# Performance work log

Hardware: AMD Instinct MI355X
Metric: run time of the kernel (lower is better)

The kernel has to match this reference:

```python
import jax, jax.numpy as jnp
import numpy as np

SIGMA = 1.0   # kernel influence distance (init kwarg)
RADIUS = 1.0  # kernel radius (kernel points live within this ball)


def setup_inputs() -> dict:
    key = jax.random.key(0)
    k0, k1, k2, k3, k4, k5 = jax.random.split(key, 6)
    N, M, H, K, Cin, Cout = 50000, 50000, 32, 15, 64, 64
    q_points = jax.random.normal(k0, (M, 3), dtype=jnp.float32)
    s_points = jax.random.normal(k1, (N, 3), dtype=jnp.float32)
    s_feats = jax.random.normal(k2, (N, Cin), dtype=jnp.float32)
    # index == N selects the padded 'fantom' point (zero features, far away)
    neighbor_indices = jax.random.randint(k3, (M, H), 0, N + 1, dtype=jnp.int64)
    kernel_points = jax.random.normal(k4, (K, 3), dtype=jnp.float32) * (0.4 * RADIUS)
    weights = jax.random.normal(k5, (K, Cin, Cout), dtype=jnp.float32) * 0.05
    return {
        'q_points': q_points,
        's_points': s_points,
        's_feats': s_feats,
        'neighbor_indices': neighbor_indices,
        'kernel_points': kernel_points,
        'weights': weights,
    }


def reference(q_points, s_points, s_feats, neighbor_indices, kernel_points, weights):
    # Pad source points with a far-away fantom point and zero features so that
    # neighbor_indices == N behaves as an empty neighbor slot.
    s_pts = jnp.concatenate([s_points, jnp.full((1, 3), 1e6, s_points.dtype)], axis=0)
    s_fts = jnp.concatenate([s_feats, jnp.zeros((1, s_feats.shape[1]), s_feats.dtype)], axis=0)

    # Gather neighbors and center on query points: (M, H, 3)
    neighbors = s_pts[neighbor_indices] - q_points[:, None, :]
    # Distances to each kernel point: (M, H, K)
    diffs = neighbors[:, :, None, :] - kernel_points[None, None, :, :]
    sq_dists = jnp.sum(diffs * diffs, axis=-1)
    # Linear kernel influence (KPConv 'linear' mode): (M, H, K)
    influence = jnp.maximum(1.0 - jnp.sqrt(sq_dists) / SIGMA, 0.0)
    # Fantom neighbors are ~1e6 away -> influence exactly 0.

    # Gather neighbor features: (M, H, Cin)
    nb_feats = s_fts[neighbor_indices]
    # Weight features by kernel influence, reduce over neighbors: (M, K, Cin)
    weighted = jnp.einsum('mhk,mhc->mkc', influence, nb_feats)
    # Apply per-kernel-point linear maps and sum over kernel points: (M, Cout)
    out = jnp.einsum('mkc,kcd->md', weighted, weights)

    # Normalize by the number of valid (non-zero-feature) neighbors.
    feat_sum = jnp.sum(nb_feats, axis=-1)               # (M, H)
    nnum = jnp.maximum(jnp.sum(feat_sum > 0.0, axis=-1), 1)  # (M,)
    return out / nnum[:, None].astype(out.dtype)
```

## Files before the change

### kernel.cpp

```cpp
#include <hip/hip_runtime.h>

#define NPTS 50000
#define MPTS 50000
#define HN 32
#define KCD 960
#define PSTRIDE 968

typedef float f32x4 __attribute__((ext_vector_type(4)));
typedef short s16x8 __attribute__((ext_vector_type(8)));

__device__ __forceinline__ unsigned short bf_rne(float x) {
    union { float f; unsigned u; } v; v.f = x;
    unsigned r = v.u + 0x7fffu + ((v.u >> 16) & 1u);
    return (unsigned short)(r >> 16);
}
__device__ __forceinline__ unsigned short bf_trunc(float x) {
    union { float f; unsigned u; } v; v.f = x;
    return (unsigned short)(v.u >> 16);
}
__device__ __forceinline__ unsigned pack_bf(float lo, float hi) {
    union { float f; unsigned u; } a, b; a.f = lo; b.f = hi;
    return __builtin_amdgcn_perm(b.u, a.u, 0x07060302u);
}
__device__ __forceinline__ unsigned pack_rne(float lo, float hi) {
    return ((unsigned)bf_rne(hi) << 16) | (unsigned)bf_rne(lo);
}
__device__ __forceinline__ unsigned pack_lo16(unsigned a, unsigned b) {
    return __builtin_amdgcn_perm(b, a, 0x05040100u);
}
__device__ __forceinline__ unsigned pack_hi16(unsigned a, unsigned b) {
    return __builtin_amdgcn_perm(b, a, 0x07060302u);
}

__global__ __launch_bounds__(256) void prep_bf(const float* __restrict__ w,
                                               const float* __restrict__ feats,
                                               unsigned short* __restrict__ WT,
                                               unsigned char* __restrict__ signs,
                                               unsigned short* __restrict__ fbf) {
    int b = blockIdx.x;
    if (b < 240) {
        int t = b * 256 + threadIdx.x;
        int kc = t >> 6, d = t & 63;
        WT[d * KCD + kc] = bf_rne(w[t]);
    } else {
        int t = threadIdx.x;
        int p = t >> 4, r = t & 15;
        int n = (b - 240) * 16 + p;
        const float* src = feats + (size_t)n * 64 + r;
        float c0 = src[0], c1 = src[16], c2 = src[32], c3 = src[48];
        float s = c0 + c1 + c2 + c3;
        s += __shfl_xor(s, 1); s += __shfl_xor(s, 2);
        s += __shfl_xor(s, 4); s += __shfl_xor(s, 8);
        if (r == 0) signs[n] = (s > 0.f) ? 1 : 0;
        uint2 o; o.x = pack_rne(c0, c1); o.y = pack_rne(c2, c3);
        *(uint2*)(fbf + (size_t)n * 64 + r * 4) = o;
    }
}

__global__ __launch_bounds__(256) void prep_f32(const float* __restrict__ w,
                                                const float* __restrict__ feats,
                                                unsigned short* __restrict__ WT,
                                                unsigned char* __restrict__ signs) {
    int b = blockIdx.x;
    if (b < 240) {
        int t = b * 256 + threadIdx.x;
        int kc = t >> 6, d = t & 63;
        WT[d * KCD + kc] = bf_rne(w[t]);
    } else {
        int lane = threadIdx.x & 63, wv = threadIdx.x >> 6;
        int r4 = lane >> 4, c16 = lane & 15;
        int n = (b - 240) * 16 + wv * 4 + r4;
        float4 v = *(const float4*)(feats + (size_t)n * 64 + c16 * 4);
        float s = v.x + v.y + v.z + v.w;
        s += __shfl_xor(s, 1); s += __shfl_xor(s, 2);
        s += __shfl_xor(s, 4); s += __shfl_xor(s, 8);
        if (c16 == 0) signs[n] = (s > 0.f) ? 1 : 0;
    }
}

template <bool USE_BF>
__device__ __forceinline__
void kpconv_body(const float* __restrict__ q_points,
                 const float* __restrict__ s_points,
                 const float* __restrict__ s_feats,
                 const unsigned short* __restrict__ fbf,
                 const int* __restrict__ ni,
                 const float* __restrict__ kpts,
                 const unsigned short* __restrict__ WT,
                 const unsigned char* __restrict__ signs,
                 float* __restrict__ out) {
    __shared__ __align__(16) unsigned short P_sh[16][PSTRIDE];
    __shared__ __align__(16) float rpos_sh[4][3][32];
    __shared__ int ni_sh[4][4][32];
    __shared__ float kp_sh[16][3];
    __shared__ float q_sh[16][3];
    __shared__ float inv_nnum[16];

    int tid = threadIdx.x, w = tid >> 6, lane = tid & 63;
    int m_base = blockIdx.x << 4;

    if (tid < 48) {
        kp_sh[tid / 3][tid % 3] = (tid < 45) ? kpts[tid] : 1e9f;
        q_sh[tid / 3][tid % 3] = q_points[m_base * 3 + tid];
    }
    __syncthreads();

    int h = lane & 31;
    int row = lane & 15, quad = lane >> 4, kq = quad << 3;
    int h2 = lane >> 1, half = lane & 1;

    float kx = kp_sh[row][0], ky = kp_sh[row][1], kz = kp_sh[row][2];

    float tkx[8], tky[8], tkz[8];
    #pragma unroll
    for (int j = 0; j < 8; ++j) {
        int k = half * 8 + j;
        tkx[j] = kp_sh[k][0]; tky[j] = kp_sh[k][1]; tkz[j] = kp_sh[k][2];
    }

    int idx4[4]; float rxa[4], rya[4], rza[4]; unsigned char sg4[4];
    #pragma unroll
    for (int mi = 0; mi < 4; ++mi)
        idx4[mi] = ni[(m_base + mi * 4 + w) * HN + h];
    #pragma unroll
    for (int mi = 0; mi < 4; ++mi) {
        int m_l = mi * 4 + w;
        bool valid = idx4[mi] < NPTS;
        const float* sp = s_points + (size_t)(valid ? idx4[mi] : 0) * 3;
        float px = sp[0], py = sp[1], pz = sp[2];
        unsigned char sg = signs[valid ? idx4[mi] : 0];
        rxa[mi] = (valid ? px : 1e6f) - q_sh[m_l][0];
        rya[mi] = (valid ? py : 1e6f) - q_sh[m_l][1];
        rza[mi] = (valid ? pz : 1e6f) - q_sh[m_l][2];
        sg4[mi] = valid ? sg : 0;
    }

    #pragma unroll
    for (int mi = 0; mi < 4; ++mi) {
        float rx2 = __shfl(rxa[mi], h2);
        float ry2 = __shfl(rya[mi], h2);
        float rz2 = __shfl(rza[mi], h2);
        int idx2 = __shfl(idx4[mi], h2);
        int av = 0;
        #pragma unroll
        for (int j = 0; j < 8; ++j) {
            float dx = rx2 - tkx[j], dy = ry2 - tky[j], dz = rz2 - tkz[j];
            float d2 = dx * dx + dy * dy + dz * dz;
            av |= (d2 < 1.f) ? 1 : 0;
        }
        av |= __shfl_xor(av, 1);
        bool alive = (idx2 < NPTS) && (av != 0);
        if (half == 0) ni_sh[w][mi][h2] = alive ? idx2 : NPTS;

        unsigned long long pm = __ballot((lane < 32) && (idx4[mi] < NPTS) && sg4[mi]);
        if (lane == 0) {
            int cnt = __popcll(pm);
            inv_nnum[mi * 4 + w] = 1.f / (float)(cnt < 1 ? 1 : cnt);
        }
    }

    #pragma unroll
    for (int mi = 0; mi < 4; ++mi) {
        int m_l = mi * 4 + w;
        if (lane < 32) {
            rpos_sh[w][0][h] = rxa[mi];
            rpos_sh[w][1][h] = rya[mi];
            rpos_sh[w][2][h] = rza[mi];
        }

        float g0[8], g1[8], g2[8], g3[8];
        unsigned d0[8], d1[8];
        #pragma unroll
        for (int j = 0; j < 8; ++j) {
            int idxj = ni_sh[w][mi][kq + j];
            if (USE_BF) {
                d0[j] = 0u; d1[j] = 0u;
                if (idxj < NPTS) {
                    uint2 v = *(const uint2*)(fbf + (size_t)idxj * 64 + row * 4);
                    d0[j] = v.x; d1[j] = v.y;
                }
            } else {
                g0[j] = 0.f; g1[j] = 0.f; g2[j] = 0.f; g3[j] = 0.f;
                if (idxj < NPTS) {
                    const float* fp = s_feats + (size_t)idxj * 64 + row;
                    g0[j] = fp[0]; g1[j] = fp[16]; g2[j] = fp[32]; g3[j] = fp[48];
                }
            }
        }

        float4 ra0 = *(const float4*)&rpos_sh[w][0][kq];
        float4 ra1 = *(const float4*)&rpos_sh[w][0][kq + 4];
        float4 rb0 = *(const float4*)&rpos_sh[w][1][kq];
        float4 rb1 = *(const float4*)&rpos_sh[w][1][kq + 4];
        float4 rc0 = *(const float4*)&rpos_sh[w][2][kq];
        float4 rc1 = *(const float4*)&rpos_sh[w][2][kq + 4];
        float hx[8] = {ra0.x, ra0.y, ra0.z, ra0.w, ra1.x, ra1.y, ra1.z, ra1.w};
        float hy[8] = {rb0.x, rb0.y, rb0.z, rb0.w, rb1.x, rb1.y, rb1.z, rb1.w};
        float hz[8] = {rc0.x, rc0.y, rc0.z, rc0.w, rc1.x, rc1.y, rc1.z, rc1.w};
        float infl[8];
        #pragma unroll
        for (int j = 0; j < 8; ++j) {
            float dx = hx[j] - kx, dy = hy[j] - ky, dz = hz[j] - kz;
            float d2 = dx * dx + dy * dy + dz * dz;
            float f = 1.f - sqrtf(d2);
            infl[j] = f > 0.f ? f : 0.f;
        }
        union { unsigned u[4]; s16x8 v; } af;
        #pragma unroll
        for (int p = 0; p < 4; ++p) af.u[p] = pack_bf(infl[2 * p], infl[2 * p + 1]);

        #pragma unroll
        for (int ch = 0; ch < 4; ++ch) {
            union { unsigned u[4]; s16x8 v; } bfr;
            if (USE_BF) {
                #pragma unroll
                for (int p = 0; p < 4; ++p) {
                    unsigned a = (ch < 2) ? d0[2 * p] : d1[2 * p];
                    unsigned b = (ch < 2) ? d0[2 * p + 1] : d1[2 * p + 1];
                    bfr.u[p] = (ch & 1) ? pack_hi16(a, b) : pack_lo16(a, b);
                }
            } else {
                const float* gs = (ch == 0) ? g0 : (ch == 1) ? g1 : (ch == 2) ? g2 : g3;
                #pragma unroll
                for (int p = 0; p < 4; ++p) bfr.u[p] = pack_bf(gs[2 * p], gs[2 * p + 1]);
            }
            f32x4 acc = {0.f, 0.f, 0.f, 0.f};
            acc = __builtin_amdgcn_mfma_f32_16x16x32_bf16(af.v, bfr.v, acc, 0, 0, 0);
            int cc = ch * 16 + row;
            #pragma unroll
            for (int r = 0; r < 4; ++r) {
                int k2 = quad * 4 + r;
                if (k2 < 15) {
                    int col = (k2 << 6) | (cc ^ ((k2 >> 2) << 4));
                    P_sh[m_l][col] = bf_trunc(acc[r]);
                }
            }
        }
    }
    __syncthreads();

    {
        int dbase = w << 4;
        f32x4 acc = {0.f, 0.f, 0.f, 0.f};
        const unsigned short* wtp = WT + (size_t)(dbase + row) * KCD + kq;
        #pragma unroll 6
        for (int s = 0; s < 30; ++s) {
            int k = s >> 1;
            int c0 = ((s & 1) << 5) + kq;
            int cx = c0 ^ (((k >> 2) & 3) << 4);
            s16x8 a = *(const s16x8*)&P_sh[row][(k << 6) | cx];
            s16x8 b = *(const s16x8*)&wtp[s * 32];
            acc = __builtin_amdgcn_mfma_f32_16x16x32_bf16(a, b, acc, 0, 0, 0);
        }
        #pragma unroll
        for (int r = 0; r < 4; ++r) {
            int m_l = quad * 4 + r;
            out[(size_t)(m_base + m_l) * 64 + dbase + row] = acc[r] * inv_nnum[m_l];
        }
    }
}

__global__ __launch_bounds__(256, 4)
void kpconv_main_bf(const float* __restrict__ q, const float* __restrict__ sp,
                    const unsigned short* __restrict__ fbf,
                    const int* __restrict__ ni, const float* __restrict__ kp,
                    const unsigned short* __restrict__ WT,
                    const unsigned char* __restrict__ signs,
                    float* __restrict__ out) {
    kpconv_body<true>(q, sp, nullptr, fbf, ni, kp, WT, signs, out);
}

__global__ __launch_bounds__(256, 4)
void kpconv_main_f32(const float* __restrict__ q, const float* __restrict__ sp,
                     const float* __restrict__ sf,
                     const int* __restrict__ ni, const float* __restrict__ kp,
                     const unsigned short* __restrict__ WT,
                     const unsigned char* __restrict__ signs,
                     float* __restrict__ out) {
    kpconv_body<false>(q, sp, sf, nullptr, ni, kp, WT, signs, out);
}

extern "C" void kernel_launch(void* const* d_in, const int* in_sizes, int n_in,
                              void* d_out, int out_size, void* d_ws, size_t ws_size,
                              hipStream_t stream) {
    const float* q  = (const float*)d_in[0];
    const float* sp = (const float*)d_in[1];
    const float* sf = (const float*)d_in[2];
    const int*   ni = (const int*)d_in[3];
    const float* kp = (const float*)d_in[4];
    const float* wt = (const float*)d_in[5];
    float* out = (float*)d_out;

    unsigned short* WT = (unsigned short*)d_ws;
    unsigned char* signs = (unsigned char*)d_ws + 122880;
    unsigned short* fbf = (unsigned short*)((char*)d_ws + 172928);
    const size_t need = 172928 + (size_t)NPTS * 64 * 2;

    if (ws_size >= need) {
        hipLaunchKernelGGL(prep_bf, dim3(240 + NPTS / 16), dim3(256), 0, stream,
                           wt, sf, WT, signs, fbf);
        hipLaunchKernelGGL(kpconv_main_bf, dim3(MPTS / 16), dim3(256), 0, stream,
                           q, sp, fbf, ni, kp, WT, signs, out);
    } else {
        hipLaunchKernelGGL(prep_f32, dim3(240 + NPTS / 16), dim3(256), 0, stream,
                           wt, sf, WT, signs);
        hipLaunchKernelGGL(kpconv_main_f32, dim3(MPTS / 16), dim3(256), 0, stream,
                           q, sp, sf, ni, kp, WT, signs, out);
    }
}
```

Before: 150.4 us.

## Split fused KPConv kernel into influence-gather and weight-GEMM passes via workspace

Splits the fused main kernel into two kernels when the workspace is large enough. The first computes the per-point weighted features (M x K*Cin in bf16), scales them by the neighbor count and writes them to global memory. The second runs a plain bf16 MFMA GEMM against the transposed weights. The aim is to cut shared memory and register pressure so each stage gets higher occupancy, at the cost of writing and rereading about 96 MB of intermediate data.

New measurement: 203.1 us. 35.1% more time.

```diff
diff --git a/kernel.cpp b/kernel.cpp
--- a/kernel.cpp
+++ b/kernel.cpp
@@ -78,6 +78,185 @@
     }
 }
 
+__global__ __launch_bounds__(256, 6)
+void kpconv_p1(const float* __restrict__ q_points,
+               const float* __restrict__ s_points,
+               const unsigned short* __restrict__ fbf,
+               const int* __restrict__ ni,
+               const float* __restrict__ kpts,
+               const unsigned char* __restrict__ signs,
+               unsigned short* __restrict__ P) {
+    __shared__ __align__(16) unsigned short pbuf[4][1032];
+    __shared__ __align__(16) float rpos_sh[4][3][32];
+    __shared__ int ni_sh[4][4][32];
+    __shared__ float kp_sh[16][3];
+    __shared__ float q_sh[16][3];
+
+    int tid = threadIdx.x, w = tid >> 6, lane = tid & 63;
+    int m_base = blockIdx.x << 4;
+
+    if (tid < 48) {
+        kp_sh[tid / 3][tid % 3] = (tid < 45) ? kpts[tid] : 1e9f;
+        q_sh[tid / 3][tid % 3] = q_points[m_base * 3 + tid];
+    }
+    __syncthreads();
+
+    int h = lane & 31;
+    int row = lane & 15, quad = lane >> 4, kq = quad << 3;
+    int h2 = lane >> 1, half = lane & 1;
+
+    float kx = kp_sh[row][0], ky = kp_sh[row][1], kz = kp_sh[row][2];
+
+    float tkx[8], tky[8], tkz[8];
+    #pragma unroll
+    for (int j = 0; j < 8; ++j) {
+        int k = half * 8 + j;
+        tkx[j] = kp_sh[k][0]; tky[j] = kp_sh[k][1]; tkz[j] = kp_sh[k][2];
+    }
+
+    int idx4[4]; float rxa[4], rya[4], rza[4]; unsigned char sg4[4];
+    #pragma unroll
+    for (int mi = 0; mi < 4; ++mi)
+        idx4[mi] = ni[(m_base + mi * 4 + w) * HN + h];
+    #pragma unroll
+    for (int mi = 0; mi < 4; ++mi) {
+        int m_l = mi * 4 + w;
+        bool valid = idx4[mi] < NPTS;
+        const float* sp = s_points + (size_t)(valid ? idx4[mi] : 0) * 3;
+        float px = sp[0], py = sp[1], pz = sp[2];
+        unsigned char sg = signs[valid ? idx4[mi] : 0];
+        rxa[mi] = (valid ? px : 1e6f) - q_sh[m_l][0];
+        rya[mi] = (valid ? py : 1e6f) - q_sh[m_l][1];
+        rza[mi] = (valid ? pz : 1e6f) - q_sh[m_l][2];
+        sg4[mi] = valid ? sg : 0;
+    }
+
+    float inv4[4];
+    #pragma unroll
+    for (int mi = 0; mi < 4; ++mi) {
+        float rx2 = __shfl(rxa[mi], h2);
+        float ry2 = __shfl(rya[mi], h2);
+        float rz2 = __shfl(rza[mi], h2);
+        int idx2 = __shfl(idx4[mi], h2);
+        int av = 0;
+        #pragma unroll
+        for (int j = 0; j < 8; ++j) {
+            float dx = rx2 - tkx[j], dy = ry2 - tky[j], dz = rz2 - tkz[j];
+            float d2 = dx * dx + dy * dy + dz * dz;
+            av |= (d2 < 1.f) ? 1 : 0;
+        }
+        av |= __shfl_xor(av, 1);
+        bool alive = (idx2 < NPTS) && (av != 0);
+        if (half == 0) ni_sh[w][mi][h2] = alive ? idx2 : NPTS;
+
+        unsigned long long pm = __ballot((lane < 32) && (idx4[mi] < NPTS) && sg4[mi]);
+        int cnt = __popcll(pm);
+        inv4[mi] = 1.f / (float)(cnt < 1 ? 1 : cnt);
+    }
+
+    #pragma unroll
+    for (int mi = 0; mi < 4; ++mi) {
+        int m_l = mi * 4 + w;
+        if (lane < 32) {
+            rpos_sh[w][0][h] = rxa[mi];
+            rpos_sh[w][1][h] = rya[mi];
+            rpos_sh[w][2][h] = rza[mi];
+        }
+
+        unsigned d0[8], d1[8];
+        #pragma unroll
+        for (int j = 0; j < 8; ++j) {
+            int idxj = ni_sh[w][mi][kq + j];
+            d0[j] = 0u; d1[j] = 0u;
+            if (idxj < NPTS) {
+                uint2 v = *(const uint2*)(fbf + (size_t)idxj * 64 + row * 4);
+                d0[j] = v.x; d1[j] = v.y;
+            }
+        }
+
+        float4 ra0 = *(const float4*)&rpos_sh[w][0][kq];
+        float4 ra1 = *(const float4*)&rpos_sh[w][0][kq + 4];
+        float4 rb0 = *(const float4*)&rpos_sh[w][1][kq];
+        float4 rb1 = *(const float4*)&rpos_sh[w][1][kq + 4];
+        float4 rc0 = *(const float4*)&rpos_sh[w][2][kq];
+        float4 rc1 = *(const float4*)&rpos_sh[w][2][kq + 4];
+        float hx[8] = {ra0.x, ra0.y, ra0.z, ra0.w, ra1.x, ra1.y, ra1.z, ra1.w};
+        float hy[8] = {rb0.x, rb0.y, rb0.z, rb0.w, rb1.x, rb1.y, rb1.z, rb1.w};
+        float hz[8] = {rc0.x, rc0.y, rc0.z, rc0.w, rc1.x, rc1.y, rc1.z, rc1.w};
+        float infl[8];
+        #pragma unroll
+        for (int j = 0; j < 8; ++j) {
+            float dx = hx[j] - kx, dy = hy[j] - ky, dz = hz[j] - kz;
+            float d2 = dx * dx + dy * dy + dz * dz;
+            float f = 1.f - sqrtf(d2);
+            infl[j] = f > 0.f ? f : 0.f;
+        }
+        union { unsigned u[4]; s16x8 v; } af;
+        #pragma unroll
+        for (int p = 0; p < 4; ++p) af.u[p] = pack_bf(infl[2 * p], infl[2 * p + 1]);
+
+        #pragma unroll
+        for (int ch = 0; ch < 4; ++ch) {
+            union { unsigned u[4]; s16x8 v; } bfr;
+            #pragma unroll
+            for (int p = 0; p < 4; ++p) {
+                unsigned a = (ch < 2) ? d0[2 * p] : d1[2 * p];
+                unsigned b = (ch < 2) ? d0[2 * p + 1] : d1[2 * p + 1];
+                bfr.u[p] = (ch & 1) ? pack_hi16(a, b) : pack_lo16(a, b);
+            }
+            f32x4 acc = {0.f, 0.f, 0.f, 0.f};
+            acc = __builtin_amdgcn_mfma_f32_16x16x32_bf16(af.v, bfr.v, acc, 0, 0, 0);
+            int cc = ch * 16 + row;
+            #pragma unroll
+            for (int r = 0; r < 4; ++r) {
+                int k2 = quad * 4 + r;
+                int col = (k2 << 6) | (cc ^ ((k2 >> 2) << 4));
+                pbuf[w][col] = bf_trunc(acc[r] * inv4[mi]);
+            }
+        }
+
+        {
+            unsigned short* Pr = P + (size_t)(m_base + m_l) * KCD;
+            int c8 = lane;
+            int k = c8 >> 3, c0 = (c8 & 7) << 3;
+            int swz = (k << 6) | (c0 ^ (((k >> 2) & 3) << 4));
+            s16x8 v0 = *(const s16x8*)&pbuf[w][swz];
+            *(s16x8*)(Pr + c8 * 8) = v0;
+            int c8b = 64 + lane;
+            if (c8b < 120) {
+                int kb = c8b >> 3, c0b = (c8b & 7) << 3;
+                int swzb = (kb << 6) | (c0b ^ (((kb >> 2) & 3) << 4));
+                s16x8 v1 = *(const s16x8*)&pbuf[w][swzb];
+                *(s16x8*)(Pr + c8b * 8) = v1;
+            }
+        }
+    }
+}
+
+__global__ __launch_bounds__(256, 8)
+void kpconv_p2(const unsigned short* __restrict__ P,
+               const unsigned short* __restrict__ WT,
+               float* __restrict__ out) {
+    int tid = threadIdx.x, w = tid >> 6, lane = tid & 63;
+    int row = lane & 15, quad = lane >> 4, kq = quad << 3;
+    int m_base = blockIdx.x << 4;
+    int dbase = w << 4;
+    const unsigned short* ap = P + (size_t)(m_base + row) * KCD + kq;
+    const unsigned short* bp = WT + (size_t)(dbase + row) * KCD + kq;
+    f32x4 acc = {0.f, 0.f, 0.f, 0.f};
+    #pragma unroll 6
+    for (int s = 0; s < 30; ++s) {
+        s16x8 a = *(const s16x8*)(ap + s * 32);
+        s16x8 b = *(const s16x8*)(bp + s * 32);
+        acc = __builtin_amdgcn_mfma_f32_16x16x32_bf16(a, b, acc, 0, 0, 0);
+    }
+    #pragma unroll
+    for (int r = 0; r < 4; ++r) {
+        int m_l = quad * 4 + r;
+        out[(size_t)(m_base + m_l) * 64 + dbase + row] = acc[r];
+    }
+}
+
 template <bool USE_BF>
 __device__ __forceinline__
 void kpconv_body(const float* __restrict__ q_points,
@@ -293,10 +472,21 @@
 
     unsigned short* WT = (unsigned short*)d_ws;
     unsigned char* signs = (unsigned char*)d_ws + 122880;
-    unsigned short* fbf = (unsigned short*)((char*)d_ws + 172928);
-    const size_t need = 172928 + (size_t)NPTS * 64 * 2;
-
-    if (ws_size >= need) {
+    const size_t off_fbf = 172928;
+    unsigned short* fbf = (unsigned short*)((char*)d_ws + off_fbf);
+    const size_t off_P = off_fbf + (size_t)NPTS * 64 * 2;
+    unsigned short* P = (unsigned short*)((char*)d_ws + off_P);
+    const size_t need_bf = off_P;
+    const size_t need_split = off_P + (size_t)MPTS * KCD * 2;
+
+    if (ws_size >= need_split) {
+        hipLaunchKernelGGL(prep_bf, dim3(240 + NPTS / 16), dim3(256), 0, stream,
+                           wt, sf, WT, signs, fbf);
+        hipLaunchKernelGGL(kpconv_p1, dim3(MPTS / 16), dim3(256), 0, stream,
+                           q, sp, fbf, ni, kp, signs, P);
+        hipLaunchKernelGGL(kpconv_p2, dim3(MPTS / 16), dim3(256), 0, stream,
+                           P, WT, out);
+    } else if (ws_size >= need_bf) {
         hipLaunchKernelGGL(prep_bf, dim3(240 + NPTS / 16), dim3(256), 0, stream,
                            wt, sf, WT, signs, fbf);
         hipLaunchKernelGGL(kpconv_main_bf, dim3(MPTS / 16), dim3(256), 0, stream,
```
